# Performance work log

Measured on AMD Instinct MI355X. Metric: run time of the kernel, lower is better.

## Reference

```python
import jax, jax.numpy as jnp
import numpy as np

N, F, E, FE, H, OUT = 20000, 128, 320000, 16, 128, 128
NTYPES = 2  # types = (0, 1)
NPAIRS = NTYPES * NTYPES


def setup_inputs() -> dict:
    key = jax.random.key(0)
    ks = jax.random.split(key, 12)
    edge_in_dim = 2 * F + FE
    node_in_dim = F + H
    s = lambda *shape: 1.0 / np.sqrt(shape[-2])
    return {
        "x": jax.random.normal(ks[0], (N, 1, F), dtype=jnp.float32),
        "edge_index": jax.random.randint(ks[1], (2, E), 0, N, dtype=jnp.int64),
        "edge_attr": jax.random.normal(ks[2], (E, FE), dtype=jnp.float32),
        "node_type": jax.random.randint(ks[3], (N,), 0, NTYPES, dtype=jnp.int64),
        # edge MLP params, stacked over the 4 (t1,t2) type pairs
        "ew1": jax.random.normal(ks[4], (NPAIRS, edge_in_dim, H), dtype=jnp.float32) * (1.0 / np.sqrt(edge_in_dim)),
        "eb1": jnp.zeros((NPAIRS, H), dtype=jnp.float32),
        "ew2": jax.random.normal(ks[5], (NPAIRS, H, H), dtype=jnp.float32) * (1.0 / np.sqrt(H)),
        "eb2": jnp.zeros((NPAIRS, H), dtype=jnp.float32),
        # node MLP params, stacked over the 2 node types
        "nw1": jax.random.normal(ks[6], (NTYPES, node_in_dim, H), dtype=jnp.float32) * (1.0 / np.sqrt(node_in_dim)),
        "nb1": jnp.zeros((NTYPES, H), dtype=jnp.float32),
        "nw2": jax.random.normal(ks[7], (NTYPES, H, OUT), dtype=jnp.float32) * (1.0 / np.sqrt(H)),
        "nb2": jnp.zeros((NTYPES, OUT), dtype=jnp.float32),
    }


def reference(x, edge_index, edge_attr, node_type, ew1, eb1, ew2, eb2, nw1, nb1, nw2, nb2):
    x0 = x[:, 0]  # [N, F]
    row, col = edge_index[0], edge_index[1]

    # ---- edge model: type-pair-dispatched 2-layer ReLU MLP ----
    edge_in = jnp.concatenate([x0[row], x0[col], edge_attr], axis=-1)  # [E, 2F+FE]
    h1 = jax.nn.relu(jnp.einsum("ei,pih->eph", edge_in, ew1) + eb1)    # [E, P, H]
    h2 = jax.nn.relu(jnp.einsum("eph,phk->epk", h1, ew2) + eb2)        # [E, P, H]
    pair_id = node_type[row] * NTYPES + node_type[col]                  # [E]
    pair_oh = jax.nn.one_hot(pair_id, NPAIRS, dtype=h2.dtype)           # [E, P]
    edge_feat = jnp.einsum("epk,ep->ek", h2, pair_oh)                   # [E, H]

    # ---- aggregation: sum over incoming edges per source (row) node ----
    agg = jax.ops.segment_sum(edge_feat, row, num_segments=N)           # [N, H]

    # ---- node model: type-dispatched 2-layer MLP + residual ----
    node_in = jnp.concatenate([x0, agg], axis=-1)                       # [N, F+H]
    n1 = jax.nn.relu(jnp.einsum("ni,tih->nth", node_in, nw1) + nb1)     # [N, T, H]
    n2 = jnp.einsum("nth,thk->ntk", n1, nw2) + nb2                      # [N, T, OUT]
    type_oh = jax.nn.one_hot(node_type, NTYPES, dtype=n2.dtype)         # [N, T]
    out = jnp.einsum("ntk,nt->nk", n2, type_oh)                         # [N, OUT]
    out = out + x0[:, :OUT]  # residual
    return out[:, None, :]  # [N, 1, OUT]
```

## Files before the change

### kernel.cpp

```cpp
#include <hip/hip_runtime.h>

#define N_NODES 20000
#define N_EDGES 320000
#define NBINS   (4*N_NODES)
#define SCAN_NBLK 313

typedef unsigned short u16;
typedef __attribute__((ext_vector_type(8))) short bf16x8;
typedef __attribute__((ext_vector_type(4))) float f32x4;
typedef __attribute__((ext_vector_type(4))) unsigned int u32x4;

__device__ __forceinline__ float b2f(u16 b){
  unsigned u = ((unsigned)b) << 16; float f; __builtin_memcpy(&f, &u, 4); return f;
}
__device__ __forceinline__ u16 f2b(float f){
  unsigned u; __builtin_memcpy(&u, &f, 4); u += 0x7FFF + ((u >> 16) & 1); return (u16)(u >> 16);
}

#define NX   (N_NODES*128)
#define NW1T (4*320*128)
#define NW2T (4*128*128)
#define NN1  (2*256*128)
#define NN2  (2*128*128)

__global__ void k_preconv(const float* __restrict__ x,
                          const float* __restrict__ ew1, const float* __restrict__ ew2,
                          const float* __restrict__ nw1, const float* __restrict__ nw2,
                          u16* __restrict__ x0b,
                          u16* __restrict__ wt1t, u16* __restrict__ wt2t,
                          u16* __restrict__ nw1t, u16* __restrict__ nw2t)
{
  int t = blockIdx.x * 256 + threadIdx.x;
  if (t < NX) { x0b[t] = f2b(x[t]); return; }
  t -= NX;
  if (t < NW1T) {
    int p = t / 40960, r = t % 40960; int k = r >> 7, n = r & 127;
    float v = (k < 272) ? ew1[(p * 272 + k) * 128 + n] : 0.f;
    wt1t[(p * 128 + n) * 320 + k] = f2b(v);
    return;
  }
  t -= NW1T;
  if (t < NW2T) {
    int p = t >> 14, r = t & 16383; int k = r >> 7, n = r & 127;
    wt2t[(p * 128 + n) * 128 + k] = f2b(ew2[(p * 128 + k) * 128 + n]);
    return;
  }
  t -= NW2T;
  if (t < NN1) {
    int ty = t >> 15, r = t & 32767; int k = r >> 7, n = r & 127;
    nw1t[(ty * 128 + n) * 256 + k] = f2b(nw1[(ty * 256 + k) * 128 + n]);
    return;
  }
  t -= NN1;
  if (t < NN2) {
    int ty = t >> 14, r = t & 16383; int k = r >> 7, n = r & 127;
    nw2t[(ty * 128 + n) * 128 + k] = f2b(nw2[(ty * 128 + k) * 128 + n]);
  }
}

__global__ void k_hist(const int* __restrict__ ei, const int* __restrict__ ntp,
                       int* __restrict__ hist, int* __restrict__ hist_nt,
                       u16* __restrict__ srank)
{
  int t = blockIdx.x * 256 + threadIdx.x;
  int lane = threadIdx.x & 63;
  if (t < N_EDGES) {
    int r = ei[t], c = ei[N_EDGES + t];
    int tr = ntp[r], tc = ntp[c];
    int key = (tr * 2 + tc) * N_NODES + r;
    int rk = atomicAdd(&hist[key], 1);
    srank[t] = (u16)rk;
  }
  bool valid = t < N_NODES;
  int ty = valid ? ntp[t] : -1;
  unsigned long long m0 = __ballot(ty == 0);
  unsigned long long m1 = __ballot(ty == 1);
  if (lane == 0) {
    int c0 = __popcll(m0), c1 = __popcll(m1);
    if (c0) atomicAdd(&hist_nt[0], c0);
    if (c1) atomicAdd(&hist_nt[1], c1);
  }
}

__global__ void k_scan1(const int* __restrict__ hist, int* __restrict__ parts)
{
  __shared__ int s[256];
  int i = blockIdx.x * 256 + threadIdx.x;
  s[threadIdx.x] = (i < NBINS) ? hist[i] : 0;
  __syncthreads();
  for (int off = 128; off > 0; off >>= 1) {
    if (threadIdx.x < off) s[threadIdx.x] += s[threadIdx.x + off];
    __syncthreads();
  }
  if (threadIdx.x == 0) parts[blockIdx.x] = s[0];
}

__global__ void k_scan2(int* __restrict__ parts)
{
  __shared__ int s[512];
  int t = threadIdx.x;
  int v = (t < SCAN_NBLK) ? parts[t] : 0;
  s[t] = v; __syncthreads();
  for (int off = 1; off < 512; off <<= 1) {
    int xv = (t >= off) ? s[t - off] : 0;
    __syncthreads();
    s[t] += xv;
    __syncthreads();
  }
  if (t < SCAN_NBLK) parts[t] = s[t] - v;
}

__global__ void k_scan3(const int* __restrict__ hist, const int* __restrict__ parts,
                        int* __restrict__ bstart)
{
  __shared__ int s[256];
  int i = blockIdx.x * 256 + threadIdx.x;
  int v = (i < NBINS) ? hist[i] : 0;
  s[threadIdx.x] = v; __syncthreads();
  for (int off = 1; off < 256; off <<= 1) {
    int xv = (threadIdx.x >= off) ? s[threadIdx.x - off] : 0;
    __syncthreads();
    s[threadIdx.x] += xv;
    __syncthreads();
  }
  int excl = s[threadIdx.x] - v + parts[blockIdx.x];
  if (i < NBINS) bstart[i] = excl;
  if (i == 0) bstart[NBINS] = N_EDGES;
}

__global__ void k_place(const int* __restrict__ ei, const int* __restrict__ ntp,
                        const u16* __restrict__ srank, const int* __restrict__ bstart,
                        int2* __restrict__ sedge,
                        int* __restrict__ cur_nt, const int* __restrict__ hist_nt,
                        int* __restrict__ nidx)
{
  int t = blockIdx.x * 256 + threadIdx.x;
  int lane = threadIdx.x & 63;
  if (t < N_EDGES) {
    int r = ei[t], c = ei[N_EDGES + t];
    int tr = ntp[r], tc = ntp[c];
    int key = (tr * 2 + tc) * N_NODES + r;
    int pos = bstart[key] + (int)srank[t];
    int2 v; v.x = r | (c << 15); v.y = t;
    sedge[pos] = v;
  }
  bool valid = t < N_NODES;
  int ty = valid ? ntp[t] : -1;
  unsigned long long m0 = __ballot(ty == 0);
  unsigned long long m1 = __ballot(ty == 1);
  int b0 = 0, b1 = 0;
  if (lane == 0) {
    int c0 = __popcll(m0), c1 = __popcll(m1);
    if (c0) b0 = atomicAdd(&cur_nt[0], c0);
    if (c1) b1 = atomicAdd(&cur_nt[1], c1);
  }
  b0 = __shfl(b0, 0); b1 = __shfl(b1, 0);
  if (valid) {
    unsigned long long lt = (1ull << lane) - 1ull;
    int pos = (ty == 0) ? (b0 + __popcll(m0 & lt))
                        : (hist_nt[0] + b1 + __popcll(m1 & lt));
    nidx[pos] = t;
  }
}

__launch_bounds__(512, 2)
__global__ void k_edge(const u16* __restrict__ x0b, const float* __restrict__ ea,
                       const u16* __restrict__ wt1t, const u16* __restrict__ wt2t,
                       const float* __restrict__ eb1, const float* __restrict__ eb2,
                       const int* __restrict__ bstart, const int2* __restrict__ sedge,
                       u16* __restrict__ h2s)
{
  __shared__ u16 sEIN[2 * 256 * 72];
  __shared__ u16 sW1[2 * 128 * 72];
  __shared__ u16 sW2[128 * 136];
  __shared__ float sEb1[128];
  __shared__ float sEb2[128];
  __shared__ int sRow[256];
  __shared__ int sCol[256];
  __shared__ int sEid[256];

  const int p    = blockIdx.y;
  const int tid  = threadIdx.x;
  const int lane = tid & 63;
  const int wid  = tid >> 6;
  const int wr   = wid >> 1;
  const int wc   = wid & 1;
  const int llo  = lane & 15;
  const int lhi  = lane >> 4;
  const int rr   = tid >> 1;
  const int sub  = tid & 1;
  const int wn   = tid & 127;
  const int wkq  = (tid >> 7) & 3;

  const int base_p = bstart[p * N_NODES];
  const int end_p  = bstart[(p + 1) * N_NODES];

  for (int i = tid; i < 128 * 128; i += 512) {
    int n = i >> 7, k = i & 127;
    sW2[n * 136 + k] = wt2t[(p * 128 + n) * 128 + k];
  }
  if (tid < 128) { sEb1[tid] = eb1[p * 128 + tid]; sEb2[tid] = eb2[p * 128 + tid]; }

  const u16* wbase = wt1t + (p * 128 + wn) * 320 + wkq * 16;

  for (int ts = base_p + blockIdx.x * 256; ts < end_p; ts += gridDim.x * 256) {
    const int cnt = min(256, end_p - ts);
    if (tid < 256) {
      int2 v = {0, 0};
      if (tid < cnt) v = sedge[ts + tid];
      sRow[tid] = v.x & 32767; sCol[tid] = v.x >> 15; sEid[tid] = v.y;
    }
    __syncthreads();
    const int myRow = sRow[rr], myCol = sCol[rr], myEid = sEid[rr];

    {
      u32x4 ld[4], lw[2];
      const u16* src = &x0b[myRow * 128 + sub * 32];
      #pragma unroll
      for (int j = 0; j < 4; ++j) ld[j] = *(const u32x4*)(src + j * 8);
      #pragma unroll
      for (int j = 0; j < 2; ++j) lw[j] = *(const u32x4*)(wbase + j * 8);
      u16* dE = &sEIN[rr * 72 + sub * 32];
      #pragma unroll
      for (int j = 0; j < 4; ++j) *(u32x4*)(dE + j * 8) = ld[j];
      u16* dW = &sW1[wn * 72 + wkq * 16];
      #pragma unroll
      for (int j = 0; j < 2; ++j) *(u32x4*)(dW + j * 8) = lw[j];
    }
    __syncthreads();

    f32x4 acc[4][4];
    #pragma unroll
    for (int i = 0; i < 4; ++i)
      #pragma unroll
      for (int j = 0; j < 4; ++j)
        acc[i][j] = (f32x4){0.f, 0.f, 0.f, 0.f};

    #pragma unroll
    for (int ch = 0; ch < 5; ++ch) {
      const int cur = ch & 1;
      u32x4 ldE[4], ldW[2];
      if (ch < 4) {
        const int cn = ch + 1;
        if (cn < 4) {
          const int node = (cn < 2) ? myRow : myCol;
          const u16* src = &x0b[node * 128 + (cn & 1) * 64 + sub * 32];
          #pragma unroll
          for (int j = 0; j < 4; ++j) ldE[j] = *(const u32x4*)(src + j * 8);
        } else {
          #pragma unroll
          for (int j = 0; j < 4; ++j) ldE[j] = (u32x4){0u, 0u, 0u, 0u};
          if (sub == 0) {
            const float* src = &ea[myEid * 16];
            float v[16];
            #pragma unroll
            for (int j = 0; j < 4; ++j) {
              f32x4 f = *(const f32x4*)(src + j * 4);
              v[j*4+0]=f[0]; v[j*4+1]=f[1]; v[j*4+2]=f[2]; v[j*4+3]=f[3];
            }
            #pragma unroll
            for (int w = 0; w < 4; ++w)
              ldE[0][w] = (unsigned)f2b(v[2*w]) | ((unsigned)f2b(v[2*w+1]) << 16);
            #pragma unroll
            for (int w = 0; w < 4; ++w)
              ldE[1][w] = (unsigned)f2b(v[8+2*w]) | ((unsigned)f2b(v[9+2*w]) << 16);
          }
        }
        #pragma unroll
        for (int j = 0; j < 2; ++j) ldW[j] = *(const u32x4*)(wbase + cn * 64 + j * 8);
      }
      #pragma unroll
      for (int ks = 0; ks < 2; ++ks) {
        const int kk = ks * 32 + lhi * 8;
        bf16x8 a[4], b[4];
        #pragma unroll
        for (int i = 0; i < 4; ++i)
          a[i] = *(const bf16x8*)&sEIN[cur * (256 * 72) + (wr * 64 + i * 16 + llo) * 72 + kk];
        #pragma unroll
        for (int j = 0; j < 4; ++j)
          b[j] = *(const bf16x8*)&sW1[cur * (128 * 72) + (wc * 64 + j * 16 + llo) * 72 + kk];
        #pragma unroll
        for (int i = 0; i < 4; ++i)
          #pragma unroll
          for (int j = 0; j < 4; ++j)
            acc[i][j] = __builtin_amdgcn_mfma_f32_16x16x32_bf16(a[i], b[j], acc[i][j], 0, 0, 0);
      }
      if (ch < 4) {
        const int nb = cur ^ 1;
        u16* dE = &sEIN[nb * (256 * 72) + rr * 72 + sub * 32];
        #pragma unroll
        for (int j = 0; j < 4; ++j) *(u32x4*)(dE + j * 8) = ldE[j];
        u16* dW = &sW1[nb * (128 * 72) + wn * 72 + wkq * 16];
        #pragma unroll
        for (int j = 0; j < 2; ++j) *(u32x4*)(dW + j * 8) = ldW[j];
      }
      __syncthreads();
    }

    u16* sH1 = sEIN;
    #pragma unroll
    for (int i = 0; i < 4; ++i) {
      #pragma unroll
      for (int j = 0; j < 4; ++j) {
        const int c = wc * 64 + j * 16 + llo;
        const float bias = sEb1[c];
        #pragma unroll
        for (int r = 0; r < 4; ++r) {
          const int m = wr * 64 + i * 16 + lhi * 4 + r;
          float v = acc[i][j][r] + bias;
          v = v > 0.f ? v : 0.f;
          sH1[m * 136 + c] = f2b(v);
        }
      }
    }
    __syncthreads();

    #pragma unroll
    for (int i = 0; i < 4; ++i)
      #pragma unroll
      for (int j = 0; j < 4; ++j)
        acc[i][j] = (f32x4){0.f, 0.f, 0.f, 0.f};

    #pragma unroll
    for (int ck = 0; ck < 4; ++ck) {
      const int kk = ck * 32 + lhi * 8;
      bf16x8 a[4], b[4];
      #pragma unroll
      for (int i = 0; i < 4; ++i)
        a[i] = *(const bf16x8*)&sH1[(wr * 64 + i * 16 + llo) * 136 + kk];
      #pragma unroll
      for (int j = 0; j < 4; ++j)
        b[j] = *(const bf16x8*)&sW2[(wc * 64 + j * 16 + llo) * 136 + kk];
      #pragma unroll
      for (int i = 0; i < 4; ++i)
        #pragma unroll
        for (int j = 0; j < 4; ++j)
          acc[i][j] = __builtin_amdgcn_mfma_f32_16x16x32_bf16(a[i], b[j], acc[i][j], 0, 0, 0);
    }

    #pragma unroll
    for (int i = 0; i < 4; ++i) {
      #pragma unroll
      for (int j = 0; j < 4; ++j) {
        const int c = wc * 64 + j * 16 + llo;
        const float bias = sEb2[c];
        #pragma unroll
        for (int r = 0; r < 4; ++r) {
          const int m = wr * 64 + i * 16 + lhi * 4 + r;
          if (m < cnt) {
            float v = acc[i][j][r] + bias;
            v = v > 0.f ? v : 0.f;
            h2s[(ts + m) * 128 + c] = f2b(v);
          }
        }
      }
    }
    __syncthreads();
  }
}

__launch_bounds__(512, 2)
__global__ void k_node(const u16* __restrict__ x0b, const float* __restrict__ xf,
                       const u16* __restrict__ h2s,
                       const u16* __restrict__ nw1t, const u16* __restrict__ nw2t,
                       const float* __restrict__ nb1, const float* __restrict__ nb2,
                       const int* __restrict__ bstart,
                       const int* __restrict__ nidx, const int* __restrict__ hist_nt,
                       float* __restrict__ out)
{
  const int ty    = blockIdx.y;
  const int cnt0  = hist_nt[0];
  const int cnt_t = ty ? (N_NODES - cnt0) : cnt0;
  const int t0    = blockIdx.x * 64;
  if (t0 >= cnt_t) return;
  const int base_t = ty ? cnt0 : 0;

  __shared__ u16 sNIN[64 * 264];
  __shared__ u16 sNW1[128 * 264];
  __shared__ u16 sNW2[128 * 136];
  __shared__ float sNb1[128];
  __shared__ float sNb2[128];
  __shared__ int sNid[64];

  const int tid  = threadIdx.x;
  const int lane = tid & 63;
  const int wid  = tid >> 6;
  const int llo  = lane & 15;
  const int lhi  = lane >> 4;
  const int cnt  = min(64, cnt_t - t0);

  for (int i = tid; i < 128 * 256; i += 512) {
    int n = i >> 8, k = i & 255;
    sNW1[n * 264 + k] = nw1t[(ty * 128 + n) * 256 + k];
  }
  for (int i = tid; i < 128 * 128; i += 512) {
    int n = i >> 7, k = i & 127;
    sNW2[n * 136 + k] = nw2t[(ty * 128 + n) * 128 + k];
  }
  if (tid < 128) { sNb1[tid] = nb1[ty * 128 + tid]; sNb2[tid] = nb2[ty * 128 + tid]; }
  if (tid < 64) {
    int nid = 0;
    if (tid < cnt) nid = nidx[base_t + t0 + tid];
    sNid[tid] = nid;
  }
  __syncthreads();

  {
    const int m = tid >> 3, q = tid & 7;
    const int nid = sNid[m];
    const u16* xs = &x0b[nid * 128 + q * 16];
    u16* dst = &sNIN[m * 264 + q * 16];
    #pragma unroll
    for (int j = 0; j < 2; ++j) *(u32x4*)(dst + j * 8) = *(const u32x4*)(xs + j * 8);

    float a[16];
    #pragma unroll
    for (int j = 0; j < 16; ++j) a[j] = 0.f;
    #pragma unroll
    for (int pr = 0; pr < 2; ++pr) {
      const int key = (ty * 2 + pr) * N_NODES + nid;
      const int s = bstart[key], e = bstart[key + 1];
      for (int pos = s; pos < e; ++pos) {
        const u16* hp = &h2s[pos * 128 + q * 16];
        #pragma unroll
        for (int j = 0; j < 2; ++j) {
          u32x4 v = *(const u32x4*)(hp + j * 8);
          #pragma unroll
          for (int w = 0; w < 4; ++w) {
            unsigned uu = v[w];
            a[j * 8 + w * 2 + 0] += b2f((u16)(uu & 0xFFFFu));
            a[j * 8 + w * 2 + 1] += b2f((u16)(uu >> 16));
          }
        }
      }
    }
    u16* ad = &sNIN[m * 264 + 128 + q * 16];
    #pragma unroll
    for (int j = 0; j < 16; ++j) ad[j] = f2b(a[j]);
  }
  __syncthreads();

  f32x4 acc[4];
  #pragma unroll
  for (int i = 0; i < 4; ++i) acc[i] = (f32x4){0.f, 0.f, 0.f, 0.f};

  #pragma unroll
  for (int ck = 0; ck < 8; ++ck) {
    const int kk = ck * 32 + lhi * 8;
    bf16x8 a[4], b;
    #pragma unroll
    for (int i = 0; i < 4; ++i)
      a[i] = *(const bf16x8*)&sNIN[(i * 16 + llo) * 264 + kk];
    b = *(const bf16x8*)&sNW1[(wid * 16 + llo) * 264 + kk];
    #pragma unroll
    for (int i = 0; i < 4; ++i)
      acc[i] = __builtin_amdgcn_mfma_f32_16x16x32_bf16(a[i], b, acc[i], 0, 0, 0);
  }
  __syncthreads();

  u16* sH1 = sNIN;
  #pragma unroll
  for (int i = 0; i < 4; ++i) {
    const int c = wid * 16 + llo;
    const float bias = sNb1[c];
    #pragma unroll
    for (int r = 0; r < 4; ++r) {
      const int m = i * 16 + lhi * 4 + r;
      float v = acc[i][r] + bias;
      v = v > 0.f ? v : 0.f;
      sH1[m * 136 + c] = f2b(v);
    }
  }
  __syncthreads();

  #pragma unroll
  for (int i = 0; i < 4; ++i) acc[i] = (f32x4){0.f, 0.f, 0.f, 0.f};

  #pragma unroll
  for (int ck = 0; ck < 4; ++ck) {
    const int kk = ck * 32 + lhi * 8;
    bf16x8 a[4], b;
    #pragma unroll
    for (int i = 0; i < 4; ++i)
      a[i] = *(const bf16x8*)&sH1[(i * 16 + llo) * 136 + kk];
    b = *(const bf16x8*)&sNW2[(wid * 16 + llo) * 136 + kk];
    #pragma unroll
    for (int i = 0; i < 4; ++i)
      acc[i] = __builtin_amdgcn_mfma_f32_16x16x32_bf16(a[i], b, acc[i], 0, 0, 0);
  }

  #pragma unroll
  for (int i = 0; i < 4; ++i) {
    const int c = wid * 16 + llo;
    const float bias = sNb2[c];
    #pragma unroll
    for (int r = 0; r < 4; ++r) {
      const int m = i * 16 + lhi * 4 + r;
      if (m < cnt) {
        const int nid = sNid[m];
        out[nid * 128 + c] = acc[i][r] + bias + xf[nid * 128 + c];
      }
    }
  }
}

extern "C" void kernel_launch(void* const* d_in, const int* in_sizes, int n_in,
                              void* d_out, int out_size, void* d_ws, size_t ws_size,
                              hipStream_t stream)
{
  const float* x   = (const float*)d_in[0];
  const int*   ei  = (const int*)d_in[1];
  const float* ea  = (const float*)d_in[2];
  const int*   ntp = (const int*)d_in[3];
  const float* ew1 = (const float*)d_in[4];
  const float* eb1 = (const float*)d_in[5];
  const float* ew2 = (const float*)d_in[6];
  const float* eb2 = (const float*)d_in[7];
  const float* nw1 = (const float*)d_in[8];
  const float* nb1 = (const float*)d_in[9];
  const float* nw2 = (const float*)d_in[10];
  const float* nb2 = (const float*)d_in[11];

  char* ws = (char*)d_ws;
  int*  hist    = (int*)(ws + 0);
  int*  hist_nt = (int*)(ws + 320000);
  int*  cur_nt  = (int*)(ws + 320008);
  int*  parts   = (int*)(ws + 320256);
  int*  bstart  = (int*)(ws + 321792);
  u16*  srank   = (u16*)(ws + 641824);
  int2* sedge   = (int2*)(ws + 1281824);
  int*  nidx    = (int*)(ws + 3841824);
  u16*  x0b     = (u16*)(ws + 3921824);
  u16*  wt1t    = (u16*)(ws + 9041824);
  u16*  wt2t    = (u16*)(ws + 9369504);
  u16*  nw1t    = (u16*)(ws + 9500576);
  u16*  nw2t    = (u16*)(ws + 9631648);
  u16*  h2s     = (u16*)(ws + 9697184);

  hipMemsetAsync(ws, 0, 320016, stream);
  k_preconv<<<11280, 256, 0, stream>>>(x, ew1, ew2, nw1, nw2, x0b, wt1t, wt2t, nw1t, nw2t);
  k_hist<<<1250, 256, 0, stream>>>(ei, ntp, hist, hist_nt, srank);
  k_scan1<<<SCAN_NBLK, 256, 0, stream>>>(hist, parts);
  k_scan2<<<1, 512, 0, stream>>>(parts);
  k_scan3<<<SCAN_NBLK, 256, 0, stream>>>(hist, parts, bstart);
  k_place<<<1250, 256, 0, stream>>>(ei, ntp, srank, bstart, sedge, cur_nt, hist_nt, nidx);
  k_edge<<<dim3(64, 4), 512, 0, stream>>>(x0b, ea, wt1t, wt2t, eb1, eb2, bstart, sedge, h2s);
  k_node<<<dim3(313, 2), 512, 0, stream>>>(x0b, x, h2s, nw1t, nw2t, nb1, nb2, bstart, nidx, hist_nt, (float*)d_out);
}
```

Measured before the change: 190.5 us.

## Keep full edge W1 resident in LDS and W2 in registers, persistent node blocks

The edge kernel now loads the whole padded first-layer weight slice for its type pair into LDS once and keeps the second-layer weight fragments in registers. Tiles shrink to 128 edges, and edge attributes are staged separately instead of through a padded K chunk, which trims the padded K from 320 to 288. This removes the per-tile weight reloads from global memory. Bias, ReLU and bf16 packing use the v_cvt_pk_bf16_f32 instruction. The node kernel becomes persistent over a 128x2 grid so node weights are loaded once per block. In exchange, register pressure and LDS use rise, and occupancy bounds drop to 1 block per CU.

```diff
diff --git a/kernel.cpp b/kernel.cpp
--- a/kernel.cpp
+++ b/kernel.cpp
@@ -9,6 +9,7 @@
 typedef __attribute__((ext_vector_type(8))) short bf16x8;
 typedef __attribute__((ext_vector_type(4))) float f32x4;
 typedef __attribute__((ext_vector_type(4))) unsigned int u32x4;
+typedef __attribute__((ext_vector_type(2))) unsigned int u32x2;
 
 __device__ __forceinline__ float b2f(u16 b){
   unsigned u = ((unsigned)b) << 16; float f; __builtin_memcpy(&f, &u, 4); return f;
@@ -16,9 +17,14 @@
 __device__ __forceinline__ u16 f2b(float f){
   unsigned u; __builtin_memcpy(&u, &f, 4); u += 0x7FFF + ((u >> 16) & 1); return (u16)(u >> 16);
 }
+__device__ __forceinline__ unsigned cvtpk(float a, float b){
+  unsigned r;
+  asm("v_cvt_pk_bf16_f32 %0, %1, %2" : "=v"(r) : "v"(a), "v"(b));
+  return r;
+}
 
 #define NX   (N_NODES*128)
-#define NW1T (4*320*128)
+#define NW1T (4*288*128)
 #define NW2T (4*128*128)
 #define NN1  (2*256*128)
 #define NN2  (2*128*128)
@@ -34,9 +40,9 @@
   if (t < NX) { x0b[t] = f2b(x[t]); return; }
   t -= NX;
   if (t < NW1T) {
-    int p = t / 40960, r = t % 40960; int k = r >> 7, n = r & 127;
+    int p = t / 36864, r = t % 36864; int k = r >> 7, n = r & 127;
     float v = (k < 272) ? ew1[(p * 272 + k) * 128 + n] : 0.f;
-    wt1t[(p * 128 + n) * 320 + k] = f2b(v);
+    wt1t[(p * 128 + n) * 288 + k] = f2b(v);
     return;
   }
   t -= NW1T;
@@ -163,203 +169,188 @@
   }
 }
 
-__launch_bounds__(512, 2)
+__launch_bounds__(512, 1)
 __global__ void k_edge(const u16* __restrict__ x0b, const float* __restrict__ ea,
                        const u16* __restrict__ wt1t, const u16* __restrict__ wt2t,
                        const float* __restrict__ eb1, const float* __restrict__ eb2,
                        const int* __restrict__ bstart, const int2* __restrict__ sedge,
                        u16* __restrict__ h2s)
 {
-  __shared__ u16 sEIN[2 * 256 * 72];
-  __shared__ u16 sW1[2 * 128 * 72];
-  __shared__ u16 sW2[128 * 136];
+  __shared__ u16 sW1[128 * 296];
+  __shared__ u16 sEIN[2 * 128 * 72];
+  __shared__ u16 sEA[128 * 40];
   __shared__ float sEb1[128];
   __shared__ float sEb2[128];
-  __shared__ int sRow[256];
-  __shared__ int sCol[256];
-  __shared__ int sEid[256];
+  __shared__ int2 sMeta[128];
 
   const int p    = blockIdx.y;
   const int tid  = threadIdx.x;
   const int lane = tid & 63;
   const int wid  = tid >> 6;
-  const int wr   = wid >> 1;
   const int wc   = wid & 1;
+  const int we   = wid >> 1;
   const int llo  = lane & 15;
   const int lhi  = lane >> 4;
-  const int rr   = tid >> 1;
-  const int sub  = tid & 1;
-  const int wn   = tid & 127;
-  const int wkq  = (tid >> 7) & 3;
+  const int eidx = tid >> 2;
+  const int q    = tid & 3;
 
   const int base_p = bstart[p * N_NODES];
   const int end_p  = bstart[(p + 1) * N_NODES];
 
-  for (int i = tid; i < 128 * 128; i += 512) {
-    int n = i >> 7, k = i & 127;
-    sW2[n * 136 + k] = wt2t[(p * 128 + n) * 128 + k];
+  for (int i = tid; i < 128 * 36; i += 512) {
+    int n = i / 36, c = i % 36;
+    *(u32x4*)&sW1[n * 296 + c * 8] = *(const u32x4*)&wt1t[(p * 128 + n) * 288 + c * 8];
   }
   if (tid < 128) { sEb1[tid] = eb1[p * 128 + tid]; sEb2[tid] = eb2[p * 128 + tid]; }
 
-  const u16* wbase = wt1t + (p * 128 + wn) * 320 + wkq * 16;
-
-  for (int ts = base_p + blockIdx.x * 256; ts < end_p; ts += gridDim.x * 256) {
-    const int cnt = min(256, end_p - ts);
-    if (tid < 256) {
+  bf16x8 w2[4][4];
+  #pragma unroll
+  for (int i = 0; i < 4; ++i)
+    #pragma unroll
+    for (int ck = 0; ck < 4; ++ck)
+      w2[i][ck] = *(const bf16x8*)&wt2t[(p * 128 + wc * 64 + i * 16 + llo) * 128 + ck * 32 + lhi * 8];
+
+  u16* sH1 = sEIN;
+
+  for (int ts = base_p + blockIdx.x * 128; ts < end_p; ts += 64 * 128) {
+    const int cnt = min(128, end_p - ts);
+    if (tid < 128) {
       int2 v = {0, 0};
       if (tid < cnt) v = sedge[ts + tid];
-      sRow[tid] = v.x & 32767; sCol[tid] = v.x >> 15; sEid[tid] = v.y;
-    }
-    __syncthreads();
-    const int myRow = sRow[rr], myCol = sCol[rr], myEid = sEid[rr];
+      sMeta[tid] = v;
+    }
+    __syncthreads();
+    const int2 me = sMeta[eidx];
+    const int myRow = me.x & 32767, myCol = me.x >> 15, myEid = me.y;
 
     {
-      u32x4 ld[4], lw[2];
-      const u16* src = &x0b[myRow * 128 + sub * 32];
-      #pragma unroll
-      for (int j = 0; j < 4; ++j) ld[j] = *(const u32x4*)(src + j * 8);
-      #pragma unroll
-      for (int j = 0; j < 2; ++j) lw[j] = *(const u32x4*)(wbase + j * 8);
-      u16* dE = &sEIN[rr * 72 + sub * 32];
-      #pragma unroll
-      for (int j = 0; j < 4; ++j) *(u32x4*)(dE + j * 8) = ld[j];
-      u16* dW = &sW1[wn * 72 + wkq * 16];
-      #pragma unroll
-      for (int j = 0; j < 2; ++j) *(u32x4*)(dW + j * 8) = lw[j];
-    }
-    __syncthreads();
-
-    f32x4 acc[4][4];
+      const u16* src = &x0b[myRow * 128 + q * 16];
+      u32x4 l0 = *(const u32x4*)src;
+      u32x4 l1 = *(const u32x4*)(src + 8);
+      u16* d = &sEIN[eidx * 72 + q * 16];
+      *(u32x4*)d = l0; *(u32x4*)(d + 8) = l1;
+      u32x4 pk = (u32x4){0u, 0u, 0u, 0u};
+      if (q < 2) {
+        f32x4 f0 = *(const f32x4*)&ea[myEid * 16 + q * 8];
+        f32x4 f1 = *(const f32x4*)&ea[myEid * 16 + q * 8 + 4];
+        pk[0] = cvtpk(f0[0], f0[1]); pk[1] = cvtpk(f0[2], f0[3]);
+        pk[2] = cvtpk(f1[0], f1[1]); pk[3] = cvtpk(f1[2], f1[3]);
+      }
+      *(u32x4*)&sEA[eidx * 40 + q * 8] = pk;
+    }
+    __syncthreads();
+
+    f32x4 acc[4][2];
     #pragma unroll
     for (int i = 0; i < 4; ++i)
       #pragma unroll
-      for (int j = 0; j < 4; ++j)
+      for (int j = 0; j < 2; ++j)
         acc[i][j] = (f32x4){0.f, 0.f, 0.f, 0.f};
 
     #pragma unroll
-    for (int ch = 0; ch < 5; ++ch) {
+    for (int ch = 0; ch < 4; ++ch) {
       const int cur = ch & 1;
-      u32x4 ldE[4], ldW[2];
-      if (ch < 4) {
-        const int cn = ch + 1;
-        if (cn < 4) {
-          const int node = (cn < 2) ? myRow : myCol;
-          const u16* src = &x0b[node * 128 + (cn & 1) * 64 + sub * 32];
-          #pragma unroll
-          for (int j = 0; j < 4; ++j) ldE[j] = *(const u32x4*)(src + j * 8);
-        } else {
-          #pragma unroll
-          for (int j = 0; j < 4; ++j) ldE[j] = (u32x4){0u, 0u, 0u, 0u};
-          if (sub == 0) {
-            const float* src = &ea[myEid * 16];
-            float v[16];
-            #pragma unroll
-            for (int j = 0; j < 4; ++j) {
-              f32x4 f = *(const f32x4*)(src + j * 4);
-              v[j*4+0]=f[0]; v[j*4+1]=f[1]; v[j*4+2]=f[2]; v[j*4+3]=f[3];
-            }
-            #pragma unroll
-            for (int w = 0; w < 4; ++w)
-              ldE[0][w] = (unsigned)f2b(v[2*w]) | ((unsigned)f2b(v[2*w+1]) << 16);
-            #pragma unroll
-            for (int w = 0; w < 4; ++w)
-              ldE[1][w] = (unsigned)f2b(v[8+2*w]) | ((unsigned)f2b(v[9+2*w]) << 16);
-          }
-        }
-        #pragma unroll
-        for (int j = 0; j < 2; ++j) ldW[j] = *(const u32x4*)(wbase + cn * 64 + j * 8);
+      u32x4 n0, n1;
+      const int cn = ch + 1;
+      if (cn < 4) {
+        const int node = (cn < 2) ? myRow : myCol;
+        const u16* src = &x0b[node * 128 + (cn & 1) * 64 + q * 16];
+        n0 = *(const u32x4*)src; n1 = *(const u32x4*)(src + 8);
       }
       #pragma unroll
       for (int ks = 0; ks < 2; ++ks) {
         const int kk = ks * 32 + lhi * 8;
-        bf16x8 a[4], b[4];
+        bf16x8 a[4], b[2];
         #pragma unroll
         for (int i = 0; i < 4; ++i)
-          a[i] = *(const bf16x8*)&sEIN[cur * (256 * 72) + (wr * 64 + i * 16 + llo) * 72 + kk];
+          a[i] = *(const bf16x8*)&sW1[(wc * 64 + i * 16 + llo) * 296 + ch * 64 + kk];
         #pragma unroll
-        for (int j = 0; j < 4; ++j)
-          b[j] = *(const bf16x8*)&sW1[cur * (128 * 72) + (wc * 64 + j * 16 + llo) * 72 + kk];
+        for (int j = 0; j < 2; ++j)
+          b[j] = *(const bf16x8*)&sEIN[cur * (128 * 72) + (we * 32 + j * 16 + llo) * 72 + kk];
         #pragma unroll
         for (int i = 0; i < 4; ++i)
           #pragma unroll
-          for (int j = 0; j < 4; ++j)
+          for (int j = 0; j < 2; ++j)
             acc[i][j] = __builtin_amdgcn_mfma_f32_16x16x32_bf16(a[i], b[j], acc[i][j], 0, 0, 0);
       }
-      if (ch < 4) {
-        const int nb = cur ^ 1;
-        u16* dE = &sEIN[nb * (256 * 72) + rr * 72 + sub * 32];
+      if (cn < 4) {
+        u16* d = &sEIN[(cur ^ 1) * (128 * 72) + eidx * 72 + q * 16];
+        *(u32x4*)d = n0; *(u32x4*)(d + 8) = n1;
+      }
+      __syncthreads();
+    }
+    {
+      const int kk = lhi * 8;
+      bf16x8 a[4], b[2];
+      #pragma unroll
+      for (int i = 0; i < 4; ++i)
+        a[i] = *(const bf16x8*)&sW1[(wc * 64 + i * 16 + llo) * 296 + 256 + kk];
+      #pragma unroll
+      for (int j = 0; j < 2; ++j)
+        b[j] = *(const bf16x8*)&sEA[(we * 32 + j * 16 + llo) * 40 + kk];
+      #pragma unroll
+      for (int i = 0; i < 4; ++i)
         #pragma unroll
-        for (int j = 0; j < 4; ++j) *(u32x4*)(dE + j * 8) = ldE[j];
-        u16* dW = &sW1[nb * (128 * 72) + wn * 72 + wkq * 16];
+        for (int j = 0; j < 2; ++j)
+          acc[i][j] = __builtin_amdgcn_mfma_f32_16x16x32_bf16(a[i], b[j], acc[i][j], 0, 0, 0);
+    }
+
+    #pragma unroll
+    for (int i = 0; i < 4; ++i) {
+      const int chb = wc * 64 + i * 16 + lhi * 4;
+      const f32x4 bb = *(const f32x4*)&sEb1[chb];
+      #pragma unroll
+      for (int j = 0; j < 2; ++j) {
+        const int edge = we * 32 + j * 16 + llo;
+        float v0 = acc[i][j][0] + bb[0]; v0 = v0 > 0.f ? v0 : 0.f;
+        float v1 = acc[i][j][1] + bb[1]; v1 = v1 > 0.f ? v1 : 0.f;
+        float v2 = acc[i][j][2] + bb[2]; v2 = v2 > 0.f ? v2 : 0.f;
+        float v3 = acc[i][j][3] + bb[3]; v3 = v3 > 0.f ? v3 : 0.f;
+        u32x2 pk; pk[0] = cvtpk(v0, v1); pk[1] = cvtpk(v2, v3);
+        *(u32x2*)&sH1[edge * 136 + chb] = pk;
+      }
+    }
+    __syncthreads();
+
+    bf16x8 bh[2][4];
+    #pragma unroll
+    for (int j = 0; j < 2; ++j)
+      #pragma unroll
+      for (int ck = 0; ck < 4; ++ck)
+        bh[j][ck] = *(const bf16x8*)&sH1[(we * 32 + j * 16 + llo) * 136 + ck * 32 + lhi * 8];
+
+    #pragma unroll
+    for (int i = 0; i < 4; ++i)
+      #pragma unroll
+      for (int j = 0; j < 2; ++j)
+        acc[i][j] = (f32x4){0.f, 0.f, 0.f, 0.f};
+    #pragma unroll
+    for (int ck = 0; ck < 4; ++ck)
+      #pragma unroll
+      for (int i = 0; i < 4; ++i)
         #pragma unroll
-        for (int j = 0; j < 2; ++j) *(u32x4*)(dW + j * 8) = ldW[j];
-      }
-      __syncthreads();
-    }
-
-    u16* sH1 = sEIN;
+        for (int j = 0; j < 2; ++j)
+          acc[i][j] = __builtin_amdgcn_mfma_f32_16x16x32_bf16(w2[i][ck], bh[j][ck], acc[i][j], 0, 0, 0);
+
     #pragma unroll
     for (int i = 0; i < 4; ++i) {
-      #pragma unroll
-      for (int j = 0; j < 4; ++j) {
-        const int c = wc * 64 + j * 16 + llo;
-        const float bias = sEb1[c];
-        #pragma unroll
-        for (int r = 0; r < 4; ++r) {
-          const int m = wr * 64 + i * 16 + lhi * 4 + r;
-          float v = acc[i][j][r] + bias;
-          v = v > 0.f ? v : 0.f;
-          sH1[m * 136 + c] = f2b(v);
-        }
-      }
-    }
-    __syncthreads();
-
-    #pragma unroll
-    for (int i = 0; i < 4; ++i)
-      #pragma unroll
-      for (int j = 0; j < 4; ++j)
-        acc[i][j] = (f32x4){0.f, 0.f, 0.f, 0.f};
-
-    #pragma unroll
-    for (int ck = 0; ck < 4; ++ck) {
-      const int kk = ck * 32 + lhi * 8;
-      bf16x8 a[4], b[4];
-      #pragma unroll
-      for (int i = 0; i < 4; ++i)
-        a[i] = *(const bf16x8*)&sH1[(wr * 64 + i * 16 + llo) * 136 + kk];
-      #pragma unroll
-      for (int j = 0; j < 4; ++j)
-        b[j] = *(const bf16x8*)&sW2[(wc * 64 + j * 16 + llo) * 136 + kk];
-      #pragma unroll
-      for (int i = 0; i < 4; ++i)
-        #pragma unroll
-        for (int j = 0; j < 4; ++j)
-          acc[i][j] = __builtin_amdgcn_mfma_f32_16x16x32_bf16(a[i], b[j], acc[i][j], 0, 0, 0);
-    }
-
-    #pragma unroll
-    for (int i = 0; i < 4; ++i) {
-      #pragma unroll
-      for (int j = 0; j < 4; ++j) {
-        const int c = wc * 64 + j * 16 + llo;
-        const float bias = sEb2[c];
-        #pragma unroll
-        for (int r = 0; r < 4; ++r) {
-          const int m = wr * 64 + i * 16 + lhi * 4 + r;
-          if (m < cnt) {
-            float v = acc[i][j][r] + bias;
-            v = v > 0.f ? v : 0.f;
-            h2s[(ts + m) * 128 + c] = f2b(v);
-          }
-        }
-      }
-    }
-    __syncthreads();
-  }
-}
-
-__launch_bounds__(512, 2)
+      const int chb = wc * 64 + i * 16 + lhi * 4;
+      const f32x4 bb = *(const f32x4*)&sEb2[chb];
+      #pragma unroll
+      for (int j = 0; j < 2; ++j) {
+        const int edge = we * 32 + j * 16 + llo;
+        float v0 = acc[i][j][0] + bb[0]; v0 = v0 > 0.f ? v0 : 0.f;
+        float v1 = acc[i][j][1] + bb[1]; v1 = v1 > 0.f ? v1 : 0.f;
+        float v2 = acc[i][j][2] + bb[2]; v2 = v2 > 0.f ? v2 : 0.f;
+        float v3 = acc[i][j][3] + bb[3]; v3 = v3 > 0.f ? v3 : 0.f;
+        u32x2 pk; pk[0] = cvtpk(v0, v1); pk[1] = cvtpk(v2, v3);
+        if (edge < cnt) *(u32x2*)&h2s[(ts + edge) * 128 + chb] = pk;
+      }
+    }
+  }
+}
+
+__launch_bounds__(512, 1)
 __global__ void k_node(const u16* __restrict__ x0b, const float* __restrict__ xf,
                        const u16* __restrict__ h2s,
                        const u16* __restrict__ nw1t, const u16* __restrict__ nw2t,
@@ -371,8 +362,6 @@
   const int ty    = blockIdx.y;
   const int cnt0  = hist_nt[0];
   const int cnt_t = ty ? (N_NODES - cnt0) : cnt0;
-  const int t0    = blockIdx.x * 64;
-  if (t0 >= cnt_t) return;
   const int base_t = ty ? cnt0 : 0;
 
   __shared__ u16 sNIN[64 * 264];
@@ -387,7 +376,6 @@
   const int wid  = tid >> 6;
   const int llo  = lane & 15;
   const int lhi  = lane >> 4;
-  const int cnt  = min(64, cnt_t - t0);
 
   for (int i = tid; i < 128 * 256; i += 512) {
     int n = i >> 8, k = i & 255;
@@ -398,109 +386,118 @@
     sNW2[n * 136 + k] = nw2t[(ty * 128 + n) * 128 + k];
   }
   if (tid < 128) { sNb1[tid] = nb1[ty * 128 + tid]; sNb2[tid] = nb2[ty * 128 + tid]; }
-  if (tid < 64) {
-    int nid = 0;
-    if (tid < cnt) nid = nidx[base_t + t0 + tid];
-    sNid[tid] = nid;
-  }
   __syncthreads();
 
-  {
-    const int m = tid >> 3, q = tid & 7;
-    const int nid = sNid[m];
-    const u16* xs = &x0b[nid * 128 + q * 16];
-    u16* dst = &sNIN[m * 264 + q * 16];
-    #pragma unroll
-    for (int j = 0; j < 2; ++j) *(u32x4*)(dst + j * 8) = *(const u32x4*)(xs + j * 8);
-
-    float a[16];
-    #pragma unroll
-    for (int j = 0; j < 16; ++j) a[j] = 0.f;
-    #pragma unroll
-    for (int pr = 0; pr < 2; ++pr) {
-      const int key = (ty * 2 + pr) * N_NODES + nid;
-      const int s = bstart[key], e = bstart[key + 1];
-      for (int pos = s; pos < e; ++pos) {
-        const u16* hp = &h2s[pos * 128 + q * 16];
-        #pragma unroll
-        for (int j = 0; j < 2; ++j) {
-          u32x4 v = *(const u32x4*)(hp + j * 8);
+  for (int t0 = blockIdx.x * 64; t0 < cnt_t; t0 += 128 * 64) {
+    const int cnt = min(64, cnt_t - t0);
+    if (tid < 64) {
+      int nid = 0;
+      if (tid < cnt) nid = nidx[base_t + t0 + tid];
+      sNid[tid] = nid;
+    }
+    __syncthreads();
+
+    {
+      const int m = tid >> 3, qq = tid & 7;
+      const int nid = sNid[m];
+      const u16* xs = &x0b[nid * 128 + qq * 16];
+      u16* dst = &sNIN[m * 264 + qq * 16];
+      #pragma unroll
+      for (int j = 0; j < 2; ++j) *(u32x4*)(dst + j * 8) = *(const u32x4*)(xs + j * 8);
+
+      float a[16];
+      #pragma unroll
+      for (int j = 0; j < 16; ++j) a[j] = 0.f;
+      #pragma unroll
+      for (int pr = 0; pr < 2; ++pr) {
+        const int key = (ty * 2 + pr) * N_NODES + nid;
+        const int s = bstart[key], e = bstart[key + 1];
+        for (int pos = s; pos < e; ++pos) {
+          const u16* hp = &h2s[pos * 128 + qq * 16];
           #pragma unroll
-          for (int w = 0; w < 4; ++w) {
-            unsigned uu = v[w];
-            a[j * 8 + w * 2 + 0] += b2f((u16)(uu & 0xFFFFu));
-            a[j * 8 + w * 2 + 1] += b2f((u16)(uu >> 16));
+          for (int j = 0; j < 2; ++j) {
+            u32x4 v = *(const u32x4*)(hp + j * 8);
+            #pragma unroll
+            for (int w = 0; w < 4; ++w) {
+              unsigned uu = v[w];
+              a[j * 8 + w * 2 + 0] += b2f((u16)(uu & 0xFFFFu));
+              a[j * 8 + w * 2 + 1] += b2f((u16)(uu >> 16));
+            }
           }
         }
       }
-    }
-    u16* ad = &sNIN[m * 264 + 128 + q * 16];
-    #pragma unroll
-    for (int j = 0; j < 16; ++j) ad[j] = f2b(a[j]);
-  }
-  __syncthreads();
-
-  f32x4 acc[4];
-  #pragma unroll
-  for (int i = 0; i < 4; ++i) acc[i] = (f32x4){0.f, 0.f, 0.f, 0.f};
-
-  #pragma unroll
-  for (int ck = 0; ck < 8; ++ck) {
-    const int kk = ck * 32 + lhi * 8;
-    bf16x8 a[4], b;
-    #pragma unroll
-    for (int i = 0; i < 4; ++i)
-      a[i] = *(const bf16x8*)&sNIN[(i * 16 + llo) * 264 + kk];
-    b = *(const bf16x8*)&sNW1[(wid * 16 + llo) * 264 + kk];
-    #pragma unroll
-    for (int i = 0; i < 4; ++i)
-      acc[i] = __builtin_amdgcn_mfma_f32_16x16x32_bf16(a[i], b, acc[i], 0, 0, 0);
-  }
-  __syncthreads();
-
-  u16* sH1 = sNIN;
-  #pragma unroll
-  for (int i = 0; i < 4; ++i) {
-    const int c = wid * 16 + llo;
-    const float bias = sNb1[c];
-    #pragma unroll
-    for (int r = 0; r < 4; ++r) {
-      const int m = i * 16 + lhi * 4 + r;
-      float v = acc[i][r] + bias;
-      v = v > 0.f ? v : 0.f;
-      sH1[m * 136 + c] = f2b(v);
-    }
-  }
-  __syncthreads();
-
-  #pragma unroll
-  for (int i = 0; i < 4; ++i) acc[i] = (f32x4){0.f, 0.f, 0.f, 0.f};
-
-  #pragma unroll
-  for (int ck = 0; ck < 4; ++ck) {
-    const int kk = ck * 32 + lhi * 8;
-    bf16x8 a[4], b;
-    #pragma unroll
-    for (int i = 0; i < 4; ++i)
-      a[i] = *(const bf16x8*)&sH1[(i * 16 + llo) * 136 + kk];
-    b = *(const bf16x8*)&sNW2[(wid * 16 + llo) * 136 + kk];
-    #pragma unroll
-    for (int i = 0; i < 4; ++i)
-      acc[i] = __builtin_amdgcn_mfma_f32_16x16x32_bf16(a[i], b, acc[i], 0, 0, 0);
-  }
-
-  #pragma unroll
-  for (int i = 0; i < 4; ++i) {
-    const int c = wid * 16 + llo;
-    const float bias = sNb2[c];
-    #pragma unroll
-    for (int r = 0; r < 4; ++r) {
-      const int m = i * 16 + lhi * 4 + r;
-      if (m < cnt) {
-        const int nid = sNid[m];
-        out[nid * 128 + c] = acc[i][r] + bias + xf[nid * 128 + c];
-      }
-    }
+      u16* ad = &sNIN[m * 264 + 128 + qq * 16];
+      #pragma unroll
+      for (int j = 0; j < 8; ++j) {
+        unsigned pk = cvtpk(a[2 * j], a[2 * j + 1]);
+        *(unsigned*)(ad + 2 * j) = pk;
+      }
+    }
+    __syncthreads();
+
+    f32x4 acc[4];
+    #pragma unroll
+    for (int i = 0; i < 4; ++i) acc[i] = (f32x4){0.f, 0.f, 0.f, 0.f};
+
+    #pragma unroll
+    for (int ck = 0; ck < 8; ++ck) {
+      const int kk = ck * 32 + lhi * 8;
+      bf16x8 a[4], b;
+      #pragma unroll
+      for (int i = 0; i < 4; ++i)
+        a[i] = *(const bf16x8*)&sNIN[(i * 16 + llo) * 264 + kk];
+      b = *(const bf16x8*)&sNW1[(wid * 16 + llo) * 264 + kk];
+      #pragma unroll
+      for (int i = 0; i < 4; ++i)
+        acc[i] = __builtin_amdgcn_mfma_f32_16x16x32_bf16(a[i], b, acc[i], 0, 0, 0);
+    }
+    __syncthreads();
+
+    u16* sH1 = sNIN;
+    #pragma unroll
+    for (int i = 0; i < 4; ++i) {
+      const int c = wid * 16 + llo;
+      const float bias = sNb1[c];
+      #pragma unroll
+      for (int r = 0; r < 4; ++r) {
+        const int m = i * 16 + lhi * 4 + r;
+        float v = acc[i][r] + bias;
+        v = v > 0.f ? v : 0.f;
+        sH1[m * 136 + c] = f2b(v);
+      }
+    }
+    __syncthreads();
+
+    #pragma unroll
+    for (int i = 0; i < 4; ++i) acc[i] = (f32x4){0.f, 0.f, 0.f, 0.f};
+
+    #pragma unroll
+    for (int ck = 0; ck < 4; ++ck) {
+      const int kk = ck * 32 + lhi * 8;
+      bf16x8 a[4], b;
+      #pragma unroll
+      for (int i = 0; i < 4; ++i)
+        a[i] = *(const bf16x8*)&sH1[(i * 16 + llo) * 136 + kk];
+      b = *(const bf16x8*)&sNW2[(wid * 16 + llo) * 136 + kk];
+      #pragma unroll
+      for (int i = 0; i < 4; ++i)
+        acc[i] = __builtin_amdgcn_mfma_f32_16x16x32_bf16(a[i], b, acc[i], 0, 0, 0);
+    }
+
+    #pragma unroll
+    for (int i = 0; i < 4; ++i) {
+      const int c = wid * 16 + llo;
+      const float bias = sNb2[c];
+      #pragma unroll
+      for (int r = 0; r < 4; ++r) {
+        const int m = i * 16 + lhi * 4 + r;
+        if (m < cnt) {
+          const int nid = sNid[m];
+          out[nid * 128 + c] = acc[i][r] + bias + xf[nid * 128 + c];
+        }
+      }
+    }
+    __syncthreads();
   }
 }
 
@@ -532,18 +529,18 @@
   int*  nidx    = (int*)(ws + 3841824);
   u16*  x0b     = (u16*)(ws + 3921824);
   u16*  wt1t    = (u16*)(ws + 9041824);
-  u16*  wt2t    = (u16*)(ws + 9369504);
-  u16*  nw1t    = (u16*)(ws + 9500576);
-  u16*  nw2t    = (u16*)(ws + 9631648);
-  u16*  h2s     = (u16*)(ws + 9697184);
+  u16*  wt2t    = (u16*)(ws + 9336736);
+  u16*  nw1t    = (u16*)(ws + 9467808);
+  u16*  nw2t    = (u16*)(ws + 9598880);
+  u16*  h2s     = (u16*)(ws + 9664416);
 
   hipMemsetAsync(ws, 0, 320016, stream);
-  k_preconv<<<11280, 256, 0, stream>>>(x, ew1, ew2, nw1, nw2, x0b, wt1t, wt2t, nw1t, nw2t);
+  k_preconv<<<11216, 256, 0, stream>>>(x, ew1, ew2, nw1, nw2, x0b, wt1t, wt2t, nw1t, nw2t);
   k_hist<<<1250, 256, 0, stream>>>(ei, ntp, hist, hist_nt, srank);
   k_scan1<<<SCAN_NBLK, 256, 0, stream>>>(hist, parts);
   k_scan2<<<1, 512, 0, stream>>>(parts);
   k_scan3<<<SCAN_NBLK, 256, 0, stream>>>(hist, parts, bstart);
   k_place<<<1250, 256, 0, stream>>>(ei, ntp, srank, bstart, sedge, cur_nt, hist_nt, nidx);
   k_edge<<<dim3(64, 4), 512, 0, stream>>>(x0b, ea, wt1t, wt2t, eb1, eb2, bstart, sedge, h2s);
-  k_node<<<dim3(313, 2), 512, 0, stream>>>(x0b, x, h2s, nw1t, nw2t, nb1, nb2, bstart, nidx, hist_nt, (float*)d_out);
-}
+  k_node<<<dim3(128, 2), 512, 0, stream>>>(x0b, x, h2s, nw1t, nw2t, nb1, nb2, bstart, nidx, hist_nt, (float*)d_out);
+}
```

New measurement: 188.0 us. Within noise of the previous version (-1.3%).
